# Kernel optimization log

Hardware: AMD Instinct MI355X
Metric: run time of the kernel (lower is better)

Reference implementation:

```python
import jax, jax.numpy as jnp
import numpy as np

N_NODES = 50000
N_EDGES = 800000
NODE_DIM = 16
EDGE_DIM = 16
HIDDEN = 128
OUT_DIM = 4
N_BLOCKS = 3  # len(layers) - 1


def setup_inputs() -> dict:
    key = jax.random.key(0)
    ks = jax.random.split(key, 12)
    s = 0.05
    x = jax.random.normal(ks[0], (N_NODES, NODE_DIM), dtype=jnp.float32)
    edge_index = jax.random.randint(ks[1], (2, N_EDGES), 0, N_NODES, dtype=jnp.int64)
    edge_attr = jax.random.normal(ks[2], (N_EDGES, EDGE_DIM), dtype=jnp.float32)
    lift_w = jax.random.normal(ks[3], (NODE_DIM, HIDDEN), dtype=jnp.float32) * s
    lift_b = jnp.zeros((HIDDEN,), dtype=jnp.float32)
    # Stacked per-block params: root linear on x_i, message linear on [x_j || e_ij]
    root_w = jax.random.normal(ks[4], (N_BLOCKS, HIDDEN, HIDDEN), dtype=jnp.float32) * s
    root_b = jnp.zeros((N_BLOCKS, HIDDEN), dtype=jnp.float32)
    msg_w = jax.random.normal(ks[5], (N_BLOCKS, HIDDEN + EDGE_DIM, HIDDEN), dtype=jnp.float32) * s
    msg_b = jnp.zeros((N_BLOCKS, HIDDEN), dtype=jnp.float32)
    proj_w = jax.random.normal(ks[6], (HIDDEN, OUT_DIM), dtype=jnp.float32) * s
    proj_b = jnp.zeros((OUT_DIM,), dtype=jnp.float32)
    return {
        "x": x, "edge_index": edge_index, "edge_attr": edge_attr,
        "lift_w": lift_w, "lift_b": lift_b,
        "root_w": root_w, "root_b": root_b,
        "msg_w": msg_w, "msg_b": msg_b,
        "proj_w": proj_w, "proj_b": proj_b,
    }


def reference(x, edge_index, edge_attr, lift_w, lift_b, root_w, root_b, msg_w, msg_b, proj_w, proj_b):
    src = edge_index[0]  # message source j
    dst = edge_index[1]  # message target i
    n = x.shape[0]
    h = x @ lift_w + lift_b  # lift: [N, H]
    n_blocks = root_w.shape[0]
    for i in range(n_blocks):  # small fixed loop over layers
        m_in = jnp.concatenate([h[src], edge_attr], axis=-1)  # [E, H+Ed]
        msg = m_in @ msg_w[i] + msg_b[i]                       # [E, H]
        agg = jax.ops.segment_sum(msg, dst, num_segments=n)    # scatter-add [N, H]
        out = h @ root_w[i] + root_b[i] + agg + h               # conv + identity skip
        # last block runs with use_activation=False
        h = jax.nn.gelu(out) if i < n_blocks - 1 else out
    return h @ proj_w + proj_b  # projection [N, OUT_DIM]
```

## Files before the change

kernel.cpp:

```cpp
#include <hip/hip_runtime.h>

#define NN 50000
#define NE 800000
#define ND 16
#define ED 16
#define H  128
#define OD 4
#define SCAN_T 512
#define KPK 288
#define LDAK 296

typedef __bf16 bf16;
typedef __attribute__((ext_vector_type(8))) __bf16 bf16x8;
typedef __attribute__((ext_vector_type(4))) float f32x4;

static __device__ __forceinline__ float bf2f(unsigned short u) {
  return __builtin_bit_cast(float, (unsigned int)u << 16);
}
static __device__ __forceinline__ unsigned short f2bfu(float f) {
  return __builtin_bit_cast(unsigned short, (bf16)f);
}
static __device__ __forceinline__ unsigned int pk2(float a, float b) {
  return (unsigned int)f2bfu(a) | ((unsigned int)f2bfu(b) << 16);
}

__global__ __launch_bounds__(256) void zero_kernel(int* __restrict__ deg,
                                                   int* __restrict__ cursor) {
  int i = blockIdx.x * 256 + threadIdx.x;
  if (i < NN) { deg[i] = 0; cursor[i] = 0; }
}

__global__ __launch_bounds__(256) void degcount_kernel(
    const int* __restrict__ ei, int* __restrict__ deg) {
  int e0 = (blockIdx.x * 256 + threadIdx.x) * 4;
  if (e0 >= NE) return;
  int4 d4 = *(const int4*)&ei[NE + e0];
  atomicAdd(&deg[d4.x], 1);
  atomicAdd(&deg[d4.y], 1);
  atomicAdd(&deg[d4.z], 1);
  atomicAdd(&deg[d4.w], 1);
}

__global__ __launch_bounds__(SCAN_T) void scan_part_kernel(
    const int* __restrict__ deg, int* __restrict__ offsets,
    int* __restrict__ tops) {
  __shared__ int s[SCAN_T];
  int t = threadIdx.x;
  int i = blockIdx.x * SCAN_T + t;
  int v = (i < NN) ? deg[i] : 0;
  s[t] = v;
  __syncthreads();
  for (int off = 1; off < SCAN_T; off <<= 1) {
    int a = (t >= off) ? s[t - off] : 0;
    __syncthreads();
    s[t] += a;
    __syncthreads();
  }
  if (i < NN) offsets[i] = s[t] - v;
  if (t == SCAN_T - 1) tops[blockIdx.x] = s[t];
}

__global__ void scan_tops_kernel(int* __restrict__ tops, int ntiles,
                                 int* __restrict__ offsets) {
  if (threadIdx.x == 0) {
    int run = 0;
    for (int b = 0; b < ntiles; ++b) { int v = tops[b]; tops[b] = run; run += v; }
    offsets[NN] = NE;
  }
}

__global__ __launch_bounds__(256) void scan_add_kernel(
    int* __restrict__ offsets, const int* __restrict__ tops) {
  int i = blockIdx.x * 256 + threadIdx.x;
  if (i < NN) offsets[i] += tops[i / SCAN_T];
}

__global__ __launch_bounds__(256) void csr_fill_kernel(
    const int* __restrict__ ei, const int* __restrict__ offsets,
    int* __restrict__ cursor, int2* __restrict__ csr) {
  int part = blockIdx.x & 7;
  int e0 = (blockIdx.x >> 3) * 1024 + threadIdx.x * 4;
  if (e0 >= NE) return;
  int4 s4 = *(const int4*)&ei[e0];
  int4 d4 = *(const int4*)&ei[NE + e0];
#pragma unroll
  for (int j = 0; j < 4; ++j) {
    int dst = (&d4.x)[j];
    if ((int)(((long long)dst * 8) / NN) == part) {
      int pos = atomicAdd(&cursor[dst], 1);
      csr[offsets[dst] + pos] = make_int2((&s4.x)[j], e0 + j);
    }
  }
}

__global__ __launch_bounds__(256) void pack_w_kernel(
    const float* __restrict__ msg_w, const float* __restrict__ root_w,
    const float* __restrict__ root_b, const float* __restrict__ msg_b,
    bf16* __restrict__ Wp) {
  int idx = blockIdx.x * 256 + threadIdx.x;
  int b = idx / (128 * KPK);
  int r = idx % (128 * KPK);
  int c = r / KPK, k = r % KPK;
  float v = 0.f;
  if (k < 128)       v = root_w[((size_t)b * 128 + k) * 128 + c];
  else if (k < 256)  v = msg_w[((size_t)b * 144 + (k - 128)) * 128 + c];
  else if (k < 272)  v = msg_w[((size_t)b * 144 + 128 + (k - 256)) * 128 + c];
  else if (k == 272) v = msg_b[(size_t)b * 128 + c];
  else if (k == 273) v = root_b[(size_t)b * 128 + c];
  Wp[idx] = (bf16)v;
}

__global__ __launch_bounds__(256) void lift_kernel(
    const float* __restrict__ x, const float* __restrict__ lw,
    const float* __restrict__ lb, bf16* __restrict__ h) {
  int idx = blockIdx.x * 256 + threadIdx.x;
  int n = idx >> 7, k = idx & 127;
  float acc = lb[k];
  const float* xr = x + (size_t)n * ND;
#pragma unroll
  for (int j = 0; j < ND; ++j) acc = fmaf(xr[j], lw[j * H + k], acc);
  h[idx] = (bf16)acc;
}

__global__ __launch_bounds__(256) void gather_ea_kernel(
    const int* __restrict__ offsets, const int2* __restrict__ csr,
    const bf16* __restrict__ h, const float* __restrict__ ea,
    bf16* __restrict__ hagg, bf16* __restrict__ stat) {
  int t = threadIdx.x;
  int node = blockIdx.x * 16 + (t >> 4);
  int li = t & 15;
  int k8 = li * 8;
  int s = offsets[node], e = offsets[node + 1];
  const int* ci = (const int*)csr;
  const unsigned short* Hu = (const unsigned short*)h;

  float acc[8];
#pragma unroll
  for (int j = 0; j < 8; ++j) acc[j] = 0.f;
  float aea = 0.f;

  int p = s;
  for (; p + 4 <= e; p += 4) {
    int s0 = ci[2 * p],     e0 = ci[2 * p + 1];
    int s1 = ci[2 * p + 2], e1 = ci[2 * p + 3];
    int s2 = ci[2 * p + 4], e2 = ci[2 * p + 5];
    int s3 = ci[2 * p + 6], e3 = ci[2 * p + 7];
    uint4 v0 = *(const uint4*)&Hu[(size_t)s0 * H + k8];
    uint4 v1 = *(const uint4*)&Hu[(size_t)s1 * H + k8];
    uint4 v2 = *(const uint4*)&Hu[(size_t)s2 * H + k8];
    uint4 v3 = *(const uint4*)&Hu[(size_t)s3 * H + k8];
    float a0 = ea[(size_t)e0 * ED + li];
    float a1 = ea[(size_t)e1 * ED + li];
    float a2 = ea[(size_t)e2 * ED + li];
    float a3 = ea[(size_t)e3 * ED + li];
#pragma unroll
    for (int j = 0; j < 4; ++j) {
      unsigned int w0 = (&v0.x)[j], w1 = (&v1.x)[j], w2 = (&v2.x)[j], w3 = (&v3.x)[j];
      acc[2 * j]     += (bf2f((unsigned short)(w0 & 0xffff)) + bf2f((unsigned short)(w1 & 0xffff)))
                      + (bf2f((unsigned short)(w2 & 0xffff)) + bf2f((unsigned short)(w3 & 0xffff)));
      acc[2 * j + 1] += (bf2f((unsigned short)(w0 >> 16)) + bf2f((unsigned short)(w1 >> 16)))
                      + (bf2f((unsigned short)(w2 >> 16)) + bf2f((unsigned short)(w3 >> 16)));
    }
    aea += (a0 + a1) + (a2 + a3);
  }
  for (; p < e; ++p) {
    int s0 = ci[2 * p], e0 = ci[2 * p + 1];
    uint4 v0 = *(const uint4*)&Hu[(size_t)s0 * H + k8];
    aea += ea[(size_t)e0 * ED + li];
#pragma unroll
    for (int j = 0; j < 4; ++j) {
      unsigned int w0 = (&v0.x)[j];
      acc[2 * j]     += bf2f((unsigned short)(w0 & 0xffff));
      acc[2 * j + 1] += bf2f((unsigned short)(w0 >> 16));
    }
  }

  uint4 o;
  o.x = pk2(acc[0], acc[1]);
  o.y = pk2(acc[2], acc[3]);
  o.z = pk2(acc[4], acc[5]);
  o.w = pk2(acc[6], acc[7]);
  *(uint4*)&((unsigned short*)hagg)[(size_t)node * H + k8] = o;

  unsigned short* S = (unsigned short*)stat;
  S[(size_t)node * 32 + li] = f2bfu(aea);
  float v2 = (li == 0) ? (float)(e - s) : (li == 1 ? 1.0f : 0.0f);
  S[(size_t)node * 32 + 16 + li] = f2bfu(v2);
}

__global__ __launch_bounds__(256) void gather_h_kernel(
    const int* __restrict__ offsets, const int2* __restrict__ csr,
    const bf16* __restrict__ h, bf16* __restrict__ hagg) {
  int t = threadIdx.x;
  int node = blockIdx.x * 16 + (t >> 4);
  int li = t & 15;
  int k8 = li * 8;
  int s = offsets[node], e = offsets[node + 1];
  const int* ci = (const int*)csr;
  const unsigned short* Hu = (const unsigned short*)h;

  float acc[8];
#pragma unroll
  for (int j = 0; j < 8; ++j) acc[j] = 0.f;

  int p = s;
  for (; p + 4 <= e; p += 4) {
    int s0 = ci[2 * p];
    int s1 = ci[2 * p + 2];
    int s2 = ci[2 * p + 4];
    int s3 = ci[2 * p + 6];
    uint4 v0 = *(const uint4*)&Hu[(size_t)s0 * H + k8];
    uint4 v1 = *(const uint4*)&Hu[(size_t)s1 * H + k8];
    uint4 v2 = *(const uint4*)&Hu[(size_t)s2 * H + k8];
    uint4 v3 = *(const uint4*)&Hu[(size_t)s3 * H + k8];
#pragma unroll
    for (int j = 0; j < 4; ++j) {
      unsigned int w0 = (&v0.x)[j], w1 = (&v1.x)[j], w2 = (&v2.x)[j], w3 = (&v3.x)[j];
      acc[2 * j]     += (bf2f((unsigned short)(w0 & 0xffff)) + bf2f((unsigned short)(w1 & 0xffff)))
                      + (bf2f((unsigned short)(w2 & 0xffff)) + bf2f((unsigned short)(w3 & 0xffff)));
      acc[2 * j + 1] += (bf2f((unsigned short)(w0 >> 16)) + bf2f((unsigned short)(w1 >> 16)))
                      + (bf2f((unsigned short)(w2 >> 16)) + bf2f((unsigned short)(w3 >> 16)));
    }
  }
  for (; p < e; ++p) {
    int s0 = ci[2 * p];
    uint4 v0 = *(const uint4*)&Hu[(size_t)s0 * H + k8];
#pragma unroll
    for (int j = 0; j < 4; ++j) {
      unsigned int w0 = (&v0.x)[j];
      acc[2 * j]     += bf2f((unsigned short)(w0 & 0xffff));
      acc[2 * j + 1] += bf2f((unsigned short)(w0 >> 16));
    }
  }

  uint4 o;
  o.x = pk2(acc[0], acc[1]);
  o.y = pk2(acc[2], acc[3]);
  o.z = pk2(acc[4], acc[5]);
  o.w = pk2(acc[6], acc[7]);
  *(uint4*)&((unsigned short*)hagg)[(size_t)node * H + k8] = o;
}

__global__ __launch_bounds__(256, 2) void gemm_mfma_kernel(
    bf16* __restrict__ h, const bf16* __restrict__ hagg,
    const bf16* __restrict__ stat, const bf16* __restrict__ Wp,
    const float* __restrict__ pw, const float* __restrict__ pb,
    float* __restrict__ out, int act) {
  __shared__ bf16 as[64 * LDAK];
  int t = threadIdx.x;
  int lane = t & 63;
  int wv = t >> 6;
  int l15 = lane & 15, g = lane >> 4;
  int c0w = wv * 32;

  bf16x8 bq[9][2];
#pragma unroll
  for (int kk = 0; kk < 9; ++kk)
#pragma unroll
    for (int ni = 0; ni < 2; ++ni)
      bq[kk][ni] = *(const bf16x8*)(Wp + (size_t)(c0w + ni * 16 + l15) * KPK + kk * 32 + g * 8);

  int m0 = blockIdx.x * 64;
#pragma unroll
  for (int i = 0; i < 9; ++i) {
    int idx = i * 256 + t;
    int r = idx / 36, seg = idx % 36;
    int node = m0 + r;
    float4 v = make_float4(0.f, 0.f, 0.f, 0.f);
    if (node < NN) {
      const bf16* src;
      if (seg < 16)      src = h    + (size_t)node * H + seg * 8;
      else if (seg < 32) src = hagg + (size_t)node * H + (seg - 16) * 8;
      else               src = stat + (size_t)node * 32 + (seg - 32) * 8;
      v = *(const float4*)src;
    }
    *(float4*)(as + r * LDAK + seg * 8) = v;
  }
  __syncthreads();

  f32x4 acc[4][2];
#pragma unroll
  for (int mi = 0; mi < 4; ++mi)
#pragma unroll
    for (int ni = 0; ni < 2; ++ni)
      acc[mi][ni] = (f32x4){0.f, 0.f, 0.f, 0.f};

#pragma unroll
  for (int kk = 0; kk < 9; ++kk) {
    bf16x8 af[4];
#pragma unroll
    for (int mi = 0; mi < 4; ++mi)
      af[mi] = *(const bf16x8*)(as + (mi * 16 + l15) * LDAK + kk * 32 + g * 8);
#pragma unroll
    for (int mi = 0; mi < 4; ++mi)
#pragma unroll
      for (int ni = 0; ni < 2; ++ni)
        acc[mi][ni] = __builtin_amdgcn_mfma_f32_16x16x32_bf16(
            af[mi], bq[kk][ni], acc[mi][ni], 0, 0, 0);
  }

  if (act) {
#pragma unroll
    for (int mi = 0; mi < 4; ++mi) {
#pragma unroll
      for (int ni = 0; ni < 2; ++ni) {
#pragma unroll
        for (int i = 0; i < 4; ++i) {
          int rloc = mi * 16 + g * 4 + i;
          int row = m0 + rloc;
          int col = c0w + ni * 16 + l15;
          if (row < NN) {
            float v = acc[mi][ni][i];
            v += bf2f(__builtin_bit_cast(unsigned short, as[rloc * LDAK + col]));
            float u = 0.7978845608028654f * (v + 0.044715f * v * v * v);
            v = 0.5f * v * (1.f + tanhf(u));
            h[(size_t)row * H + col] = (bf16)v;
          }
        }
      }
    }
  } else {
    __syncthreads();
#pragma unroll
    for (int mi = 0; mi < 4; ++mi) {
#pragma unroll
      for (int ni = 0; ni < 2; ++ni) {
#pragma unroll
        for (int i = 0; i < 4; ++i) {
          int rloc = mi * 16 + g * 4 + i;
          int col = c0w + ni * 16 + l15;
          float v = acc[mi][ni][i];
          v += bf2f(__builtin_bit_cast(unsigned short, as[rloc * LDAK + col]));
          as[rloc * LDAK + col] = (bf16)v;
        }
      }
    }
    __syncthreads();
    int row = t >> 2, o = t & 3;
    float accp = pb[o];
    const unsigned short* hr = (const unsigned short*)(as + row * LDAK);
#pragma unroll
    for (int j = 0; j < H; ++j)
      accp = fmaf(bf2f(hr[j]), pw[j * OD + o], accp);
    if (m0 + row < NN) out[(size_t)(m0 + row) * OD + o] = accp;
  }
}

extern "C" void kernel_launch(void* const* d_in, const int* in_sizes, int n_in,
                              void* d_out, int out_size, void* d_ws, size_t ws_size,
                              hipStream_t stream) {
  const float* x       = (const float*)d_in[0];
  const int*   ei      = (const int*)d_in[1];
  const float* ea      = (const float*)d_in[2];
  const float* lift_w  = (const float*)d_in[3];
  const float* lift_b  = (const float*)d_in[4];
  const float* root_w  = (const float*)d_in[5];
  const float* root_b  = (const float*)d_in[6];
  const float* msg_w   = (const float*)d_in[7];
  const float* msg_b   = (const float*)d_in[8];
  const float* proj_w  = (const float*)d_in[9];
  const float* proj_b  = (const float*)d_in[10];
  float* out = (float*)d_out;

  char* w = (char*)d_ws;
  bf16*  h      = (bf16*)w;              w += (size_t)NN * H * 2;
  bf16*  hagg   = (bf16*)w;              w += (size_t)NN * H * 2;
  bf16*  stat   = (bf16*)w;              w += (size_t)NN * 32 * 2;
  bf16*  Wp     = (bf16*)w;              w += (size_t)3 * 128 * KPK * 2;
  int2*  csr    = (int2*)w;              w += (size_t)NE * 8;
  int*   deg     = (int*)w;              w += (size_t)NN * 4;
  int*   cursor  = (int*)w;              w += (size_t)NN * 4;
  int*   offsets = (int*)w;              w += (size_t)(NN + 16) * 4;
  int*   tops    = (int*)w;

  const int ntiles = (NN + SCAN_T - 1) / SCAN_T;

  zero_kernel<<<(NN + 255) / 256, 256, 0, stream>>>(deg, cursor);
  degcount_kernel<<<(NE / 4 + 255) / 256, 256, 0, stream>>>(ei, deg);
  scan_part_kernel<<<ntiles, SCAN_T, 0, stream>>>(deg, offsets, tops);
  scan_tops_kernel<<<1, 64, 0, stream>>>(tops, ntiles, offsets);
  scan_add_kernel<<<(NN + 255) / 256, 256, 0, stream>>>(offsets, tops);
  csr_fill_kernel<<<8 * ((NE + 1023) / 1024), 256, 0, stream>>>(ei, offsets, cursor, csr);

  pack_w_kernel<<<(3 * 128 * KPK) / 256, 256, 0, stream>>>(msg_w, root_w, root_b, msg_b, Wp);
  lift_kernel<<<(NN * H) / 256, 256, 0, stream>>>(x, lift_w, lift_b, h);

  for (int b = 0; b < 3; ++b) {
    if (b == 0)
      gather_ea_kernel<<<NN / 16, 256, 0, stream>>>(offsets, csr, h, ea, hagg, stat);
    else
      gather_h_kernel<<<NN / 16, 256, 0, stream>>>(offsets, csr, h, hagg);
    gemm_mfma_kernel<<<(NN + 63) / 64, 256, 0, stream>>>(
        h, hagg, stat, Wp + (size_t)b * 128 * KPK,
        proj_w, proj_b, out, b < 2 ? 1 : 0);
  }
}
```

Measured before the change: 303.3 us.

## Merge prologue kernels, single-block scan, two tiles per GEMM block

Lift, weight packing and zeroing are merged into one prologue launch, and the three-kernel scan becomes a single 1024-thread block that scans serial per-thread chunks. The GEMM kernel now processes two 64-row tiles per block so each block loads its weight fragments into registers once for twice the rows. This cuts launch count and weight reloads but halves the GEMM grid and serialises the scan into one block, which lowers parallelism.

Result: slower. 458.2 us (+51.1%).

```diff
diff --git a/kernel.cpp b/kernel.cpp
--- a/kernel.cpp
+++ b/kernel.cpp
@@ -6,9 +6,13 @@
 #define ED 16
 #define H  128
 #define OD 4
-#define SCAN_T 512
 #define KPK 288
 #define LDAK 296
+#define SB 1024
+
+#define LIFT_B (NN * H / 256)
+#define PACK_B (3 * 128 * KPK / 256)
+#define ZERO_B ((NN + 255) / 256)
 
 typedef __bf16 bf16;
 typedef __attribute__((ext_vector_type(8))) __bf16 bf16x8;
@@ -24,10 +28,37 @@
   return (unsigned int)f2bfu(a) | ((unsigned int)f2bfu(b) << 16);
 }
 
-__global__ __launch_bounds__(256) void zero_kernel(int* __restrict__ deg,
-                                                   int* __restrict__ cursor) {
-  int i = blockIdx.x * 256 + threadIdx.x;
-  if (i < NN) { deg[i] = 0; cursor[i] = 0; }
+__global__ __launch_bounds__(256) void prologue_kernel(
+    const float* __restrict__ x, const float* __restrict__ lw,
+    const float* __restrict__ lb, bf16* __restrict__ h,
+    const float* __restrict__ msg_w, const float* __restrict__ root_w,
+    const float* __restrict__ root_b, const float* __restrict__ msg_b,
+    bf16* __restrict__ Wp, int* __restrict__ deg, int* __restrict__ cursor) {
+  int bid = blockIdx.x;
+  if (bid < LIFT_B) {
+    int idx = bid * 256 + threadIdx.x;
+    int n = idx >> 7, k = idx & 127;
+    float acc = lb[k];
+    const float* xr = x + (size_t)n * ND;
+#pragma unroll
+    for (int j = 0; j < ND; ++j) acc = fmaf(xr[j], lw[j * H + k], acc);
+    h[idx] = (bf16)acc;
+  } else if (bid < LIFT_B + PACK_B) {
+    int idx = (bid - LIFT_B) * 256 + threadIdx.x;
+    int b = idx / (128 * KPK);
+    int r = idx % (128 * KPK);
+    int c = r / KPK, k = r % KPK;
+    float v = 0.f;
+    if (k < 128)       v = root_w[((size_t)b * 128 + k) * 128 + c];
+    else if (k < 256)  v = msg_w[((size_t)b * 144 + (k - 128)) * 128 + c];
+    else if (k < 272)  v = msg_w[((size_t)b * 144 + 128 + (k - 256)) * 128 + c];
+    else if (k == 272) v = msg_b[(size_t)b * 128 + c];
+    else if (k == 273) v = root_b[(size_t)b * 128 + c];
+    Wp[idx] = (bf16)v;
+  } else {
+    int i = (bid - LIFT_B - PACK_B) * 256 + threadIdx.x;
+    if (i < NN) { deg[i] = 0; cursor[i] = 0; }
+  }
 }
 
 __global__ __launch_bounds__(256) void degcount_kernel(
@@ -41,38 +72,34 @@
   atomicAdd(&deg[d4.w], 1);
 }
 
-__global__ __launch_bounds__(SCAN_T) void scan_part_kernel(
-    const int* __restrict__ deg, int* __restrict__ offsets,
-    int* __restrict__ tops) {
-  __shared__ int s[SCAN_T];
+__global__ __launch_bounds__(SB) void scan1_kernel(
+    const int* __restrict__ deg, int* __restrict__ offsets) {
+  __shared__ int s[SB];
   int t = threadIdx.x;
-  int i = blockIdx.x * SCAN_T + t;
-  int v = (i < NN) ? deg[i] : 0;
-  s[t] = v;
+  const int per = (NN + SB - 1) / SB;
+  int base = t * per;
+  int sum = 0;
+  for (int j = 0; j < per; ++j) {
+    int i = base + j;
+    if (i < NN) sum += deg[i];
+  }
+  s[t] = sum;
   __syncthreads();
-  for (int off = 1; off < SCAN_T; off <<= 1) {
+  for (int off = 1; off < SB; off <<= 1) {
     int a = (t >= off) ? s[t - off] : 0;
     __syncthreads();
     s[t] += a;
     __syncthreads();
   }
-  if (i < NN) offsets[i] = s[t] - v;
-  if (t == SCAN_T - 1) tops[blockIdx.x] = s[t];
-}
-
-__global__ void scan_tops_kernel(int* __restrict__ tops, int ntiles,
-                                 int* __restrict__ offsets) {
-  if (threadIdx.x == 0) {
-    int run = 0;
-    for (int b = 0; b < ntiles; ++b) { int v = tops[b]; tops[b] = run; run += v; }
-    offsets[NN] = NE;
-  }
-}
-
-__global__ __launch_bounds__(256) void scan_add_kernel(
-    int* __restrict__ offsets, const int* __restrict__ tops) {
-  int i = blockIdx.x * 256 + threadIdx.x;
-  if (i < NN) offsets[i] += tops[i / SCAN_T];
+  int run = (t > 0) ? s[t - 1] : 0;
+  for (int j = 0; j < per; ++j) {
+    int i = base + j;
+    if (i < NN) {
+      offsets[i] = run;
+      run += deg[i];
+    }
+  }
+  if (t == SB - 1) offsets[NN] = NE;
 }
 
 __global__ __launch_bounds__(256) void csr_fill_kernel(
@@ -91,35 +118,6 @@
       csr[offsets[dst] + pos] = make_int2((&s4.x)[j], e0 + j);
     }
   }
-}
-
-__global__ __launch_bounds__(256) void pack_w_kernel(
-    const float* __restrict__ msg_w, const float* __restrict__ root_w,
-    const float* __restrict__ root_b, const float* __restrict__ msg_b,
-    bf16* __restrict__ Wp) {
-  int idx = blockIdx.x * 256 + threadIdx.x;
-  int b = idx / (128 * KPK);
-  int r = idx % (128 * KPK);
-  int c = r / KPK, k = r % KPK;
-  float v = 0.f;
-  if (k < 128)       v = root_w[((size_t)b * 128 + k) * 128 + c];
-  else if (k < 256)  v = msg_w[((size_t)b * 144 + (k - 128)) * 128 + c];
-  else if (k < 272)  v = msg_w[((size_t)b * 144 + 128 + (k - 256)) * 128 + c];
-  else if (k == 272) v = msg_b[(size_t)b * 128 + c];
-  else if (k == 273) v = root_b[(size_t)b * 128 + c];
-  Wp[idx] = (bf16)v;
-}
-
-__global__ __launch_bounds__(256) void lift_kernel(
-    const float* __restrict__ x, const float* __restrict__ lw,
-    const float* __restrict__ lb, bf16* __restrict__ h) {
-  int idx = blockIdx.x * 256 + threadIdx.x;
-  int n = idx >> 7, k = idx & 127;
-  float acc = lb[k];
-  const float* xr = x + (size_t)n * ND;
-#pragma unroll
-  for (int j = 0; j < ND; ++j) acc = fmaf(xr[j], lw[j * H + k], acc);
-  h[idx] = (bf16)acc;
 }
 
 __global__ __launch_bounds__(256) void gather_ea_kernel(
@@ -260,89 +258,93 @@
     for (int ni = 0; ni < 2; ++ni)
       bq[kk][ni] = *(const bf16x8*)(Wp + (size_t)(c0w + ni * 16 + l15) * KPK + kk * 32 + g * 8);
 
-  int m0 = blockIdx.x * 64;
-#pragma unroll
-  for (int i = 0; i < 9; ++i) {
-    int idx = i * 256 + t;
-    int r = idx / 36, seg = idx % 36;
-    int node = m0 + r;
-    float4 v = make_float4(0.f, 0.f, 0.f, 0.f);
-    if (node < NN) {
-      const bf16* src;
-      if (seg < 16)      src = h    + (size_t)node * H + seg * 8;
-      else if (seg < 32) src = hagg + (size_t)node * H + (seg - 16) * 8;
-      else               src = stat + (size_t)node * 32 + (seg - 32) * 8;
-      v = *(const float4*)src;
-    }
-    *(float4*)(as + r * LDAK + seg * 8) = v;
-  }
-  __syncthreads();
-
-  f32x4 acc[4][2];
-#pragma unroll
-  for (int mi = 0; mi < 4; ++mi)
-#pragma unroll
-    for (int ni = 0; ni < 2; ++ni)
-      acc[mi][ni] = (f32x4){0.f, 0.f, 0.f, 0.f};
-
-#pragma unroll
-  for (int kk = 0; kk < 9; ++kk) {
-    bf16x8 af[4];
+  for (int tt = 0; tt < 2; ++tt) {
+    int tile = blockIdx.x * 2 + tt;
+    int m0 = tile * 64;
+    if (tt) __syncthreads();
+#pragma unroll
+    for (int i = 0; i < 9; ++i) {
+      int idx = i * 256 + t;
+      int r = idx / 36, seg = idx % 36;
+      int node = m0 + r;
+      float4 v = make_float4(0.f, 0.f, 0.f, 0.f);
+      if (node < NN) {
+        const bf16* src;
+        if (seg < 16)      src = h    + (size_t)node * H + seg * 8;
+        else if (seg < 32) src = hagg + (size_t)node * H + (seg - 16) * 8;
+        else               src = stat + (size_t)node * 32 + (seg - 32) * 8;
+        v = *(const float4*)src;
+      }
+      *(float4*)(as + r * LDAK + seg * 8) = v;
+    }
+    __syncthreads();
+
+    f32x4 acc[4][2];
 #pragma unroll
     for (int mi = 0; mi < 4; ++mi)
-      af[mi] = *(const bf16x8*)(as + (mi * 16 + l15) * LDAK + kk * 32 + g * 8);
-#pragma unroll
-    for (int mi = 0; mi < 4; ++mi)
 #pragma unroll
       for (int ni = 0; ni < 2; ++ni)
-        acc[mi][ni] = __builtin_amdgcn_mfma_f32_16x16x32_bf16(
-            af[mi], bq[kk][ni], acc[mi][ni], 0, 0, 0);
-  }
-
-  if (act) {
-#pragma unroll
-    for (int mi = 0; mi < 4; ++mi) {
-#pragma unroll
-      for (int ni = 0; ni < 2; ++ni) {
-#pragma unroll
-        for (int i = 0; i < 4; ++i) {
-          int rloc = mi * 16 + g * 4 + i;
-          int row = m0 + rloc;
-          int col = c0w + ni * 16 + l15;
-          if (row < NN) {
-            float v = acc[mi][ni][i];
-            v += bf2f(__builtin_bit_cast(unsigned short, as[rloc * LDAK + col]));
-            float u = 0.7978845608028654f * (v + 0.044715f * v * v * v);
-            v = 0.5f * v * (1.f + tanhf(u));
-            h[(size_t)row * H + col] = (bf16)v;
+        acc[mi][ni] = (f32x4){0.f, 0.f, 0.f, 0.f};
+
+#pragma unroll
+    for (int kk = 0; kk < 9; ++kk) {
+      bf16x8 af[4];
+#pragma unroll
+      for (int mi = 0; mi < 4; ++mi)
+        af[mi] = *(const bf16x8*)(as + (mi * 16 + l15) * LDAK + kk * 32 + g * 8);
+#pragma unroll
+      for (int mi = 0; mi < 4; ++mi)
+#pragma unroll
+        for (int ni = 0; ni < 2; ++ni)
+          acc[mi][ni] = __builtin_amdgcn_mfma_f32_16x16x32_bf16(
+              af[mi], bq[kk][ni], acc[mi][ni], 0, 0, 0);
+    }
+
+    if (act) {
+#pragma unroll
+      for (int mi = 0; mi < 4; ++mi) {
+#pragma unroll
+        for (int ni = 0; ni < 2; ++ni) {
+#pragma unroll
+          for (int i = 0; i < 4; ++i) {
+            int rloc = mi * 16 + g * 4 + i;
+            int row = m0 + rloc;
+            int col = c0w + ni * 16 + l15;
+            if (row < NN) {
+              float v = acc[mi][ni][i];
+              v += bf2f(__builtin_bit_cast(unsigned short, as[rloc * LDAK + col]));
+              float u = 0.7978845608028654f * (v + 0.044715f * v * v * v);
+              v = 0.5f * v * (1.f + tanhf(u));
+              h[(size_t)row * H + col] = (bf16)v;
+            }
           }
         }
       }
-    }
-  } else {
-    __syncthreads();
-#pragma unroll
-    for (int mi = 0; mi < 4; ++mi) {
-#pragma unroll
-      for (int ni = 0; ni < 2; ++ni) {
-#pragma unroll
-        for (int i = 0; i < 4; ++i) {
-          int rloc = mi * 16 + g * 4 + i;
-          int col = c0w + ni * 16 + l15;
-          float v = acc[mi][ni][i];
-          v += bf2f(__builtin_bit_cast(unsigned short, as[rloc * LDAK + col]));
-          as[rloc * LDAK + col] = (bf16)v;
+    } else {
+      __syncthreads();
+#pragma unroll
+      for (int mi = 0; mi < 4; ++mi) {
+#pragma unroll
+        for (int ni = 0; ni < 2; ++ni) {
+#pragma unroll
+          for (int i = 0; i < 4; ++i) {
+            int rloc = mi * 16 + g * 4 + i;
+            int col = c0w + ni * 16 + l15;
+            float v = acc[mi][ni][i];
+            v += bf2f(__builtin_bit_cast(unsigned short, as[rloc * LDAK + col]));
+            as[rloc * LDAK + col] = (bf16)v;
+          }
         }
       }
-    }
-    __syncthreads();
-    int row = t >> 2, o = t & 3;
-    float accp = pb[o];
-    const unsigned short* hr = (const unsigned short*)(as + row * LDAK);
-#pragma unroll
-    for (int j = 0; j < H; ++j)
-      accp = fmaf(bf2f(hr[j]), pw[j * OD + o], accp);
-    if (m0 + row < NN) out[(size_t)(m0 + row) * OD + o] = accp;
+      __syncthreads();
+      int row = t >> 2, o = t & 3;
+      float accp = pb[o];
+      const unsigned short* hr = (const unsigned short*)(as + row * LDAK);
+#pragma unroll
+      for (int j = 0; j < H; ++j)
+        accp = fmaf(bf2f(hr[j]), pw[j * OD + o], accp);
+      if (m0 + row < NN) out[(size_t)(m0 + row) * OD + o] = accp;
+    }
   }
 }
 
@@ -371,26 +373,19 @@
   int*   deg     = (int*)w;              w += (size_t)NN * 4;
   int*   cursor  = (int*)w;              w += (size_t)NN * 4;
   int*   offsets = (int*)w;              w += (size_t)(NN + 16) * 4;
-  int*   tops    = (int*)w;
-
-  const int ntiles = (NN + SCAN_T - 1) / SCAN_T;
-
-  zero_kernel<<<(NN + 255) / 256, 256, 0, stream>>>(deg, cursor);
+
+  prologue_kernel<<<LIFT_B + PACK_B + ZERO_B, 256, 0, stream>>>(
+      x, lift_w, lift_b, h, msg_w, root_w, root_b, msg_b, Wp, deg, cursor);
   degcount_kernel<<<(NE / 4 + 255) / 256, 256, 0, stream>>>(ei, deg);
-  scan_part_kernel<<<ntiles, SCAN_T, 0, stream>>>(deg, offsets, tops);
-  scan_tops_kernel<<<1, 64, 0, stream>>>(tops, ntiles, offsets);
-  scan_add_kernel<<<(NN + 255) / 256, 256, 0, stream>>>(offsets, tops);
+  scan1_kernel<<<1, SB, 0, stream>>>(deg, offsets);
   csr_fill_kernel<<<8 * ((NE + 1023) / 1024), 256, 0, stream>>>(ei, offsets, cursor, csr);
-
-  pack_w_kernel<<<(3 * 128 * KPK) / 256, 256, 0, stream>>>(msg_w, root_w, root_b, msg_b, Wp);
-  lift_kernel<<<(NN * H) / 256, 256, 0, stream>>>(x, lift_w, lift_b, h);
 
   for (int b = 0; b < 3; ++b) {
     if (b == 0)
       gather_ea_kernel<<<NN / 16, 256, 0, stream>>>(offsets, csr, h, ea, hagg, stat);
     else
       gather_h_kernel<<<NN / 16, 256, 0, stream>>>(offsets, csr, h, hagg);
-    gemm_mfma_kernel<<<(NN + 63) / 64, 256, 0, stream>>>(
+    gemm_mfma_kernel<<<(NN + 127) / 128, 256, 0, stream>>>(
         h, hagg, stat, Wp + (size_t)b * 128 * KPK,
         proj_w, proj_b, out, b < 2 ? 1 : 0);
   }
```
